# Kernel optimization log

Hardware: AMD Instinct MI355X
Metric: run time of the kernel (lower is better)

The kernel has to match this reference:

```python
import jax, jax.numpy as jnp
import numpy as np

N_NODES = 100000
N_EDGES = 1600000
D_IN = 128
D_HID = 128
D_OUT = 2
BN_EPS = 1e-5


def _sage_conv(x, src, dst, W_l, b_l, W_r):
    # PyG SAGEConv (aggr='mean'): out = lin_l(mean_{j in N(i)} x_j) + lin_r(x_i)
    # messages flow src -> dst
    agg = jax.ops.segment_sum(x[src], dst, num_segments=x.shape[0])
    deg = jax.ops.segment_sum(jnp.ones((src.shape[0],), x.dtype), dst,
                              num_segments=x.shape[0])
    mean = agg / jnp.maximum(deg, 1.0)[:, None]
    return mean @ W_l + b_l + x @ W_r


def _batch_norm(x, gamma, beta):
    # training-mode BatchNorm1d math over the node dimension (biased var)
    mu = jnp.mean(x, axis=0)
    var = jnp.var(x, axis=0)
    return (x - mu) * jax.lax.rsqrt(var + BN_EPS) * gamma + beta


def setup_inputs() -> dict:
    key = jax.random.key(0)
    ks = jax.random.split(key, 10)
    s = lambda d: 1.0 / np.sqrt(d)
    x = jax.random.normal(ks[0], (N_NODES, D_IN), dtype=jnp.float32)
    edge_index = jax.random.randint(ks[1], (2, N_EDGES), 0, N_NODES, dtype=jnp.int64)
    W1l = jax.random.uniform(ks[2], (D_IN, D_HID), jnp.float32, -s(D_IN), s(D_IN))
    b1 = jax.random.uniform(ks[3], (D_HID,), jnp.float32, -s(D_IN), s(D_IN))
    W1r = jax.random.uniform(ks[4], (D_IN, D_HID), jnp.float32, -s(D_IN), s(D_IN))
    W2l = jax.random.uniform(ks[5], (D_HID, D_OUT), jnp.float32, -s(D_HID), s(D_HID))
    b2 = jax.random.uniform(ks[6], (D_OUT,), jnp.float32, -s(D_HID), s(D_HID))
    W2r = jax.random.uniform(ks[7], (D_HID, D_OUT), jnp.float32, -s(D_HID), s(D_HID))
    gamma1 = jnp.ones((D_HID,), jnp.float32)
    beta1 = jnp.zeros((D_HID,), jnp.float32)
    gamma2 = jnp.ones((D_OUT,), jnp.float32)
    beta2 = jnp.zeros((D_OUT,), jnp.float32)
    return {"x": x, "edge_index": edge_index,
            "W1l": W1l, "b1": b1, "W1r": W1r, "gamma1": gamma1, "beta1": beta1,
            "W2l": W2l, "b2": b2, "W2r": W2r, "gamma2": gamma2, "beta2": beta2}


def reference(x, edge_index, W1l, b1, W1r, gamma1, beta1,
              W2l, b2, W2r, gamma2, beta2):
    src, dst = edge_index[0], edge_index[1]
    h = _sage_conv(x, src, dst, W1l, b1, W1r)
    h = _batch_norm(h, gamma1, beta1)
    h = jax.nn.relu(h)
    # dropout in eval mode = identity
    h = _sage_conv(h, src, dst, W2l, b2, W2r)
    h = _batch_norm(h, gamma2, beta2)
    return jax.nn.log_softmax(h, axis=1)
```

## Files before the change

### kernel.cpp

```cpp
#include <hip/hip_runtime.h>
#include <hip/hip_bf16.h>
#include <math.h>


#define DH 128
#define PAD 64
#define CBITS 11
#define CNODES 2048
#define MAXBKT 128
#define BUCKETCAP 65536
#define CHUNK 4096
#define CURSTRIDE 16
#define L1BLOCKS 512

typedef short short8 __attribute__((ext_vector_type(8)));
typedef float float4v __attribute__((ext_vector_type(4)));
typedef float float2v __attribute__((ext_vector_type(2)));
typedef unsigned uint4v __attribute__((ext_vector_type(4)));

template <typename T> static __device__ __forceinline__ float tof(T v);
template <> __device__ __forceinline__ float tof<float>(float v) { return v; }
template <> __device__ __forceinline__ float tof<__hip_bfloat16>(__hip_bfloat16 v) {
  return __bfloat162float(v);
}

static __device__ __forceinline__ short f2bf_s(float f) {
  union { __hip_bfloat16 h; short s; } u;
  u.h = __float2bfloat16(f);
  return u.s;
}

static __device__ __forceinline__ float bf2f(short s) {
  union { unsigned u; float f; } c;
  c.u = ((unsigned)(unsigned short)s) << 16;
  return c.f;
}

static __device__ __forceinline__ float asf(unsigned u) {
  union { unsigned u; float f; } c;
  c.u = u;
  return c.f;
}

__global__ void k_probe(const unsigned* __restrict__ xw,
                        const unsigned* __restrict__ ew,
                        int* __restrict__ flags) {
  int t = threadIdx.x;
  unsigned wx = xw[(size_t)t * 23456 + 7];
  unsigned el = (wx >> 7) & 0xFFu;
  int sx = (el >= 0x60 && el <= 0x85) ? 1 : 0;
  unsigned we = ew[(size_t)t * 12000 + 1];
  int se = (we == 0) ? 1 : 0;
  __shared__ int c[2];
  if (t < 2) c[t] = 0;
  __syncthreads();
  atomicAdd(&c[0], sx);
  atomicAdd(&c[1], se);
  __syncthreads();
  if (t == 0) {
    flags[0] = (c[0] < 192) ? 1 : 0;
    flags[2] = (c[1] > 192) ? 1 : 0;
  }
}

template <typename FT>
static __device__ __forceinline__ void wt_one(const FT* __restrict__ W1l,
                                              const FT* __restrict__ W1r,
                                              short* __restrict__ WT, int idx) {
  int n = idx >> 8, k = idx & 255;
  float v = (k < 128) ? tof(W1l[k * 128 + n]) : tof(W1r[(k - 128) * 128 + n]);
  WT[n * 256 + (k ^ ((n & 7) << 3))] = f2bf_s(v);
}
__global__ void k_xbwt(const void* __restrict__ x, const void* __restrict__ W1l,
                       const void* __restrict__ W1r, const int* __restrict__ flags,
                       __hip_bfloat162* __restrict__ xb, short* __restrict__ WT,
                       int total2) {
  int gi = blockIdx.x * blockDim.x + threadIdx.x;
  bool f32 = flags[0] != 0;
  if (gi < 32768) {
    if (f32) wt_one<float>((const float*)W1l, (const float*)W1r, WT, gi);
    else wt_one<__hip_bfloat16>((const __hip_bfloat16*)W1l, (const __hip_bfloat16*)W1r, WT, gi);
  }
  int i = gi - 32768;
  if (i >= 0 && i < total2) {
    if (f32) {
      float2 v = ((const float2*)x)[i];
      __hip_bfloat162 o;
      o.x = __float2bfloat16(v.x);
      o.y = __float2bfloat16(v.y);
      xb[i] = o;
    } else {
      xb[i] = ((const __hip_bfloat162*)x)[i];
    }
  }
}

template <typename IT>
static __device__ __forceinline__ void part_body(
    const IT* __restrict__ es, const IT* __restrict__ ed,
    int* __restrict__ bktCur, unsigned* __restrict__ bktData,
    int E, int N, int NBKT) {
  __shared__ unsigned pkt[CHUNK];
  __shared__ unsigned char bb[CHUNK];
  __shared__ unsigned ord[CHUNK];
  __shared__ int hist[MAXBKT];
  __shared__ int lstart[MAXBKT + 1];
  __shared__ int cur[MAXBKT];
  __shared__ int gbase[MAXBKT];
  int t = threadIdx.x;
  int e0 = blockIdx.x * CHUNK;
  int nE = min(CHUNK, E - e0);
  if (nE <= 0) return;

  for (int b = t; b < MAXBKT; b += 256) { hist[b] = 0; cur[b] = 0; }
  __syncthreads();
  for (int i = t; i < nE; i += 256) {
    int s = (int)es[e0 + i], d = (int)ed[e0 + i];
    if ((unsigned)s >= (unsigned)N) s = 0;
    if ((unsigned)d >= (unsigned)N) d = 0;
    int b = d >> CBITS;
    bb[i] = (unsigned char)b;
    pkt[i] = ((unsigned)(d & (CNODES - 1)) << 17) | (unsigned)s;
    atomicAdd(&hist[b], 1);
  }
  __syncthreads();
  if (t == 0) {
    int acc = 0;
    for (int b = 0; b < NBKT; ++b) { lstart[b] = acc; acc += hist[b]; }
    lstart[NBKT] = acc;
  }
  __syncthreads();
  if (t < NBKT) {
    int c = hist[t];
    gbase[t] = (c > 0) ? atomicAdd(&bktCur[t * CURSTRIDE], c) : 0;
  }
  __syncthreads();
  for (int i = t; i < nE; i += 256) {
    int b = bb[i];
    int p = atomicAdd(&cur[b], 1);
    ord[lstart[b] + p] = pkt[i];
  }
  __syncthreads();
  for (int i = t; i < nE; i += 256) {
    int lo = 0, hi = NBKT;
    while (hi - lo > 1) { int mid = (lo + hi) >> 1; if (lstart[mid] <= i) lo = mid; else hi = mid; }
    int off = gbase[lo] + (i - lstart[lo]);
    if (off < BUCKETCAP)
      bktData[(size_t)lo * BUCKETCAP + off] = ord[i];
  }
}
__launch_bounds__(256)
__global__ void k_part(const void* __restrict__ ev, const int* __restrict__ flags,
                       int* __restrict__ bktCur, unsigned* __restrict__ bktData,
                       int E, int N, int NBKT) {
  if (flags[2]) part_body<long long>((const long long*)ev, (const long long*)ev + E,
                                     bktCur, bktData, E, N, NBKT);
  else          part_body<int>((const int*)ev, (const int*)ev + E,
                               bktCur, bktData, E, N, NBKT);
}

__launch_bounds__(256)
__global__ void k_build(const unsigned* __restrict__ bktData,
                        const int* __restrict__ bktCur,
                        int* __restrict__ deg_i, int* __restrict__ srcs_pad,
                        int N, int NBKT) {
  __shared__ int deg[256];
  int b = blockIdx.x >> 3;
  int sl = blockIdx.x & 7;
  if (b >= NBKT) return;
  int t = threadIdx.x;
  deg[t] = 0;
  __syncthreads();
  int m = min(bktCur[b * CURSTRIDE], BUCKETCAP);
  const unsigned* pp = bktData + (size_t)b * BUCKETCAP;
  for (int i = t; i < m; i += 256) {
    unsigned u = pp[i];
    int dl = u >> 17;
    if ((dl >> 8) != sl) continue;
    int r = atomicAdd(&deg[dl & 255], 1);
    if (r < PAD) {
      int node = (b << CBITS) + dl;
      srcs_pad[(size_t)node * PAD + r] = (int)(u & 0x1FFFF);
    }
  }
  __syncthreads();
  int node = (b << CBITS) + (sl << 8) + t;
  if (node < N) deg_i[node] = deg[t];
}

static __device__ __forceinline__ void accum8(float2v acc[4], uint4v u) {
#pragma unroll
  for (int i = 0; i < 4; ++i) {
    float2v p;
    p[0] = asf(u[i] << 16);
    p[1] = asf(u[i] & 0xFFFF0000u);
    acc[i] += p;
  }
}
static __device__ __forceinline__ uint4v maskv(uint4v v, int keep) {
  unsigned m = keep ? 0xFFFFFFFFu : 0u;
  uint4v r;
#pragma unroll
  for (int i = 0; i < 4; ++i) r[i] = v[i] & m;
  return r;
}
__launch_bounds__(256)
__global__ void k_gather(const unsigned* __restrict__ xbu,
                         const int* __restrict__ deg_i, const int* __restrict__ srcs_pad,
                         short* __restrict__ meanbs, int N) {
  int node = blockIdx.x * 4 + (threadIdx.x >> 6);
  int lane = threadIdx.x & 63;
  int g = lane >> 4, l = lane & 15;
  if (node >= N) return;
  int dg = deg_i[node];
  int cnt = min(dg, PAD);
  const int* sl = srcs_pad + (size_t)node * PAD;
  int srcv = sl[lane];
  srcv = ((unsigned)srcv < (unsigned)N) ? srcv : 0;
  const uint4v* xv = (const uint4v*)xbu;
  float2v acc[4];
#pragma unroll
  for (int i = 0; i < 4; ++i) acc[i] = (float2v){0.f, 0.f};

  if (cnt > 0) {
    int sA0 = __shfl(srcv, g);
    int sA1 = __shfl(srcv, 4 + g);
    int sA2 = __shfl(srcv, 8 + g);
    int sA3 = __shfl(srcv, 12 + g);
    uint4v a0 = xv[(size_t)sA0 * 16 + l];
    uint4v a1 = xv[(size_t)sA1 * 16 + l];
    uint4v a2 = xv[(size_t)sA2 * 16 + l];
    uint4v a3 = xv[(size_t)sA3 * 16 + l];
    uint4v b0, b1, b2, b3;
    bool hb = cnt > 16;
    if (hb) {
      int sB0 = __shfl(srcv, 16 + g);
      int sB1 = __shfl(srcv, 20 + g);
      int sB2 = __shfl(srcv, 24 + g);
      int sB3 = __shfl(srcv, 28 + g);
      b0 = xv[(size_t)sB0 * 16 + l];
      b1 = xv[(size_t)sB1 * 16 + l];
      b2 = xv[(size_t)sB2 * 16 + l];
      b3 = xv[(size_t)sB3 * 16 + l];
    }
    a0 = maskv(a0, g < cnt);
    a1 = maskv(a1, 4 + g < cnt);
    a2 = maskv(a2, 8 + g < cnt);
    a3 = maskv(a3, 12 + g < cnt);
    accum8(acc, a0);
    accum8(acc, a1);
    accum8(acc, a2);
    accum8(acc, a3);
    if (hb) {
      b0 = maskv(b0, 16 + g < cnt);
      b1 = maskv(b1, 20 + g < cnt);
      b2 = maskv(b2, 24 + g < cnt);
      b3 = maskv(b3, 28 + g < cnt);
      accum8(acc, b0);
      accum8(acc, b1);
      accum8(acc, b2);
      accum8(acc, b3);
    }
    for (int j = 32; j < cnt; j += 16) {
      int s0 = __shfl(srcv, j + g);
      int s1 = __shfl(srcv, j + 4 + g);
      int s2 = __shfl(srcv, j + 8 + g);
      int s3 = __shfl(srcv, j + 12 + g);
      uint4v v0 = xv[(size_t)s0 * 16 + l];
      uint4v v1 = xv[(size_t)s1 * 16 + l];
      uint4v v2 = xv[(size_t)s2 * 16 + l];
      uint4v v3 = xv[(size_t)s3 * 16 + l];
      v0 = maskv(v0, j + g < cnt);
      v1 = maskv(v1, j + 4 + g < cnt);
      v2 = maskv(v2, j + 8 + g < cnt);
      v3 = maskv(v3, j + 12 + g < cnt);
      accum8(acc, v0);
      accum8(acc, v1);
      accum8(acc, v2);
      accum8(acc, v3);
    }
  }

#pragma unroll
  for (int i = 0; i < 4; ++i) {
#pragma unroll
    for (int c = 0; c < 2; ++c) {
      acc[i][c] += __shfl_xor(acc[i][c], 16);
      acc[i][c] += __shfl_xor(acc[i][c], 32);
    }
  }
  if (g == 0) {
    float invd = 1.0f / fmaxf((float)dg, 1.0f);
    short8 o;
#pragma unroll
    for (int i = 0; i < 4; ++i) {
      o[2 * i]     = f2bf_s(acc[i][0] * invd);
      o[2 * i + 1] = f2bf_s(acc[i][1] * invd);
    }
    *(short8*)(meanbs + (size_t)node * DH + l * 8) = o;
  }
}

template <typename FT>
static __device__ __forceinline__ void layer1_body(
    const short* __restrict__ meanbs, const short* __restrict__ xbs,
    const short* __restrict__ WTs, const FT* __restrict__ b1,
    __hip_bfloat16* __restrict__ h1, float* __restrict__ st1,
    int N, int ntiles) {
  __shared__ short ldsWT[32768];
  int t = threadIdx.x;
  {
    const uint4v* src = (const uint4v*)WTs;
    uint4v* dst = (uint4v*)ldsWT;
#pragma unroll
    for (int i = 0; i < 16; ++i) dst[t + i * 256] = src[t + i * 256];
  }
  __syncthreads();

  int w = t >> 6;
  int lane = t & 63;
  int m = lane & 15;
  int quad = lane >> 4;
  int xm = (m & 7) << 3;

  float bs[8], bq[8];
#pragma unroll
  for (int c = 0; c < 8; ++c) { bs[c] = 0.f; bq[c] = 0.f; }
  float bias[8];
#pragma unroll
  for (int c = 0; c < 8; ++c) bias[c] = tof(b1[c * 16 + m]);

  for (int tt = blockIdx.x; tt < ntiles; tt += gridDim.x) {
    int rowbase = tt * 64 + w * 16;
    int arowc = min(rowbase + m, N - 1);

    short8 afrag[8];
    const short* mr = meanbs + (size_t)arowc * DH;
#pragma unroll
    for (int kt = 0; kt < 4; ++kt)
      afrag[kt] = *(const short8*)(mr + kt * 32 + quad * 8);
    const short* xr = xbs + (size_t)arowc * DH;
#pragma unroll
    for (int kt = 0; kt < 4; ++kt)
      afrag[4 + kt] = *(const short8*)(xr + kt * 32 + quad * 8);

    float4v acc[8];
#pragma unroll
    for (int c = 0; c < 8; ++c) acc[c] = (float4v){0.f, 0.f, 0.f, 0.f};

#pragma unroll
    for (int kt = 0; kt < 8; ++kt) {
      int koff = (kt * 32 + quad * 8) ^ xm;
#pragma unroll
      for (int c = 0; c < 8; ++c) {
        short8 b = *(const short8*)(ldsWT + (c * 16 + m) * 256 + koff);
        acc[c] = __builtin_amdgcn_mfma_f32_16x16x32_bf16(afrag[kt], b, acc[c], 0, 0, 0);
      }
    }

#pragma unroll
    for (int c = 0; c < 8; ++c) {
      int col = c * 16 + m;
#pragma unroll
      for (int r = 0; r < 4; ++r) {
        int ro = rowbase + quad * 4 + r;
        float v = acc[c][r] + bias[c];
        if (ro < N) {
          h1[(size_t)ro * DH + col] = __float2bfloat16(v);
          bs[c] += v;
          bq[c] += v * v;
        }
      }
    }
  }

  __syncthreads();
  float* lsum = (float*)ldsWT;
  float* lsq  = lsum + 512;
#pragma unroll
  for (int c = 0; c < 8; ++c) {
    float s = bs[c], q = bq[c];
    s += __shfl_xor(s, 16); s += __shfl_xor(s, 32);
    q += __shfl_xor(q, 16); q += __shfl_xor(q, 32);
    if (quad == 0) { lsum[w * 128 + c * 16 + m] = s; lsq[w * 128 + c * 16 + m] = q; }
  }
  __syncthreads();
  if (t < 128) {
    float s = lsum[0 * 128 + t] + lsum[1 * 128 + t] + lsum[2 * 128 + t] + lsum[3 * 128 + t];
    float q = lsq[0 * 128 + t] + lsq[1 * 128 + t] + lsq[2 * 128 + t] + lsq[3 * 128 + t];
    unsafeAtomicAdd(&st1[t], s);
    unsafeAtomicAdd(&st1[128 + t], q);
  }
}
__launch_bounds__(256)
__global__ void k_layer1(const short* __restrict__ meanbs, const short* __restrict__ xbs,
                         const short* __restrict__ WTs, const void* __restrict__ b1,
                         const int* __restrict__ flags,
                         __hip_bfloat16* __restrict__ h1, float* __restrict__ st1,
                         int N, int ntiles) {
  if (flags[0])
    layer1_body<float>(meanbs, xbs, WTs, (const float*)b1, h1, st1, N, ntiles);
  else
    layer1_body<__hip_bfloat16>(meanbs, xbs, WTs, (const __hip_bfloat16*)b1,
                                h1, st1, N, ntiles);
}

template <typename FT>
static __device__ __forceinline__ void zr_body(
    const short* __restrict__ h1s, const float* __restrict__ stats1,
    const FT* __restrict__ g1, const FT* __restrict__ be1,
    const FT* __restrict__ W2l, const FT* __restrict__ W2r,
    float4* __restrict__ zr, int N) {
  __shared__ float sc[128], sh[128];
  int t = threadIdx.x;
  if (t < 128) {
    float invN = 1.0f / (float)N;
    float mu = stats1[t] * invN;
    float var = stats1[128 + t] * invN - mu * mu;
    float a = tof(g1[t]) * rsqrtf(var + 1e-5f);
    sc[t] = a;
    sh[t] = tof(be1[t]) - mu * a;
  }
  __syncthreads();
  int lane = t & 63, w = t >> 6;
  int g = lane >> 4, l = lane & 15;
  int f0 = l * 8;
  float scl[8], shl[8], wl0[8], wl1[8], wr0[8], wr1[8];
#pragma unroll
  for (int j = 0; j < 8; ++j) {
    int f = f0 + j;
    scl[j] = sc[f];
    shl[j] = sh[f];
    wl0[j] = tof(W2l[f * 2 + 0]);
    wl1[j] = tof(W2l[f * 2 + 1]);
    wr0[j] = tof(W2r[f * 2 + 0]);
    wr1[j] = tof(W2r[f * 2 + 1]);
  }
  int gw = blockIdx.x * 4 + w;
  int nw = gridDim.x * 4;
  for (int base = gw * 4; base < N; base += nw * 4) {
    int node = base + g;
    if (node < N) {
      short8 hv = *(const short8*)(h1s + (size_t)node * DH + f0);
      float z0 = 0.f, z1 = 0.f, r0 = 0.f, r1 = 0.f;
#pragma unroll
      for (int j = 0; j < 8; ++j) {
        float v = fmaxf(bf2f(hv[j]) * scl[j] + shl[j], 0.0f);
        z0 += v * wl0[j];
        z1 += v * wl1[j];
        r0 += v * wr0[j];
        r1 += v * wr1[j];
      }
#pragma unroll
      for (int off = 8; off >= 1; off >>= 1) {
        z0 += __shfl_xor(z0, off);
        z1 += __shfl_xor(z1, off);
        r0 += __shfl_xor(r0, off);
        r1 += __shfl_xor(r1, off);
      }
      if (l == 0) zr[node] = make_float4(z0, z1, r0, r1);
    }
  }
}
__launch_bounds__(256)
__global__ void k_zr(const __hip_bfloat16* __restrict__ h1, const float* __restrict__ st1,
                     const void* g1, const void* be1, const void* W2l, const void* W2r,
                     const int* __restrict__ flags, float4* __restrict__ zr, int N) {
  if (flags[0])
    zr_body<float>((const short*)h1, st1, (const float*)g1, (const float*)be1,
                   (const float*)W2l, (const float*)W2r, zr, N);
  else
    zr_body<__hip_bfloat16>((const short*)h1, st1, (const __hip_bfloat16*)g1,
                            (const __hip_bfloat16*)be1,
                            (const __hip_bfloat16*)W2l, (const __hip_bfloat16*)W2r, zr, N);
}

template <typename FT>
static __device__ __forceinline__ void h2_body(
    const float2* __restrict__ z2, const int* __restrict__ deg_i,
    const int* __restrict__ srcs_pad, const FT* __restrict__ b2,
    float2* __restrict__ h2, float* __restrict__ stats2, int N) {
  int lane = threadIdx.x & 63, w = threadIdx.x >> 6;
  int g = lane >> 4, l = lane & 15;
  float bs0 = 0.f, bs1 = 0.f, bq0 = 0.f, bq1 = 0.f;
  float bb0 = tof(b2[0]), bb1 = tof(b2[1]);
  int gw = blockIdx.x * 4 + w;
  int nw = gridDim.x * 4;
  for (int base = gw * 4; base < N; base += nw * 4) {
    int node = base + g;
    float za = 0.f, zb = 0.f;
    int dg_true = 0;
    if (node < N) {
      dg_true = deg_i[node];
      int cnt = min(dg_true, PAD);
      const int* sl = srcs_pad + (size_t)node * PAD;
      for (int j = l; j < cnt; j += 16) {
        int sj = sl[j];
        sj = ((unsigned)sj < (unsigned)N) ? sj : 0;
        float2 v = z2[2 * sj];
        za += v.x;
        zb += v.y;
      }
    }
#pragma unroll
    for (int off = 8; off >= 1; off >>= 1) {
      za += __shfl_xor(za, off);
      zb += __shfl_xor(zb, off);
    }
    if (node < N && l == 0) {
      float dg = fmaxf((float)dg_true, 1.0f);
      float2 rw = z2[2 * node + 1];
      float h0 = za / dg + rw.x + bb0;
      float h1v = zb / dg + rw.y + bb1;
      h2[node] = make_float2(h0, h1v);
      bs0 += h0; bs1 += h1v; bq0 += h0 * h0; bq1 += h1v * h1v;
    }
  }
  bs0 += __shfl_xor(bs0, 16); bs0 += __shfl_xor(bs0, 32);
  bs1 += __shfl_xor(bs1, 16); bs1 += __shfl_xor(bs1, 32);
  bq0 += __shfl_xor(bq0, 16); bq0 += __shfl_xor(bq0, 32);
  bq1 += __shfl_xor(bq1, 16); bq1 += __shfl_xor(bq1, 32);
  __shared__ float red[4][4];
  if (lane == 0) { red[w][0] = bs0; red[w][1] = bs1; red[w][2] = bq0; red[w][3] = bq1; }
  __syncthreads();
  if (threadIdx.x < 4) {
    float a = red[0][threadIdx.x] + red[1][threadIdx.x] +
              red[2][threadIdx.x] + red[3][threadIdx.x];
    unsafeAtomicAdd(&stats2[threadIdx.x], a);
  }
}
__launch_bounds__(256)
__global__ void k_h2(const float4* __restrict__ zr, const int* __restrict__ deg_i,
                     const int* __restrict__ srcs_pad, const void* b2,
                     const int* __restrict__ flags,
                     float2* __restrict__ h2, float* __restrict__ stats2, int N) {
  if (flags[0])
    h2_body<float>((const float2*)zr, deg_i, srcs_pad, (const float*)b2, h2, stats2, N);
  else
    h2_body<__hip_bfloat16>((const float2*)zr, deg_i, srcs_pad,
                            (const __hip_bfloat16*)b2, h2, stats2, N);
}

template <typename FT>
static __device__ __forceinline__ void out_body(
    const float2* __restrict__ h2, const float* __restrict__ stats2,
    const FT* __restrict__ g2, const FT* __restrict__ be2,
    void* __restrict__ out, int N) {
  int i = blockIdx.x * blockDim.x + threadIdx.x;
  if (i >= N) return;
  float invN = 1.0f / (float)N;
  float mu0 = stats2[0] * invN, mu1 = stats2[1] * invN;
  float v0 = stats2[2] * invN - mu0 * mu0;
  float v1 = stats2[3] * invN - mu1 * mu1;
  float r0 = rsqrtf(v0 + 1e-5f), r1 = rsqrtf(v1 + 1e-5f);
  float2 h = h2[i];
  float y0 = (h.x - mu0) * r0 * tof(g2[0]) + tof(be2[0]);
  float y1 = (h.y - mu1) * r1 * tof(g2[1]) + tof(be2[1]);
  float mx = fmaxf(y0, y1);
  float lse = mx + logf(expf(y0 - mx) + expf(y1 - mx));
  float o0 = y0 - lse, o1 = y1 - lse;
  if (sizeof(FT) == 4) {
    ((float2*)out)[i] = make_float2(o0, o1);
  } else {
    __hip_bfloat162 o;
    o.x = __float2bfloat16(o0);
    o.y = __float2bfloat16(o1);
    ((__hip_bfloat162*)out)[i] = o;
  }
}
__global__ void k_out(const float2* __restrict__ h2, const float* __restrict__ stats2,
                      const void* g2, const void* be2, const int* __restrict__ flags,
                      void* __restrict__ out, int N) {
  if (flags[0]) out_body<float>(h2, stats2, (const float*)g2, (const float*)be2, out, N);
  else out_body<__hip_bfloat16>(h2, stats2, (const __hip_bfloat16*)g2,
                                (const __hip_bfloat16*)be2, out, N);
}

extern "C" void kernel_launch(void* const* d_in, const int* in_sizes, int n_in,
                              void* d_out, int out_size, void* d_ws, size_t ws_size,
                              hipStream_t stream) {
  int ix = 0, ie = 1, iW1l = 2, ib1 = 3, iW1r = 4, ig1 = 5, ibe1 = 6,
      iW2l = 7, ib2 = 8, iW2r = 9, ig2 = 10, ibe2 = 11;
  if (n_in == 12) {
    int best = -1, second = -1;
    for (int i = 0; i < 12; ++i) {
      if (best < 0 || in_sizes[i] > in_sizes[best]) { second = best; best = i; }
      else if (second < 0 || in_sizes[i] > in_sizes[second]) second = i;
    }
    ix = best; ie = second;
    int c16384 = 0, c128 = 0, c256 = 0, c2 = 0;
    for (int i = 0; i < 12; ++i) {
      if (i == ix || i == ie) continue;
      int s = in_sizes[i];
      if (s == 16384) { if (c16384++ == 0) iW1l = i; else iW1r = i; }
      else if (s == 128) { if (c128 == 0) ib1 = i; else if (c128 == 1) ig1 = i; else ibe1 = i; c128++; }
      else if (s == 256) { if (c256++ == 0) iW2l = i; else iW2r = i; }
      else { if (c2 == 0) ib2 = i; else if (c2 == 1) ig2 = i; else ibe2 = i; c2++; }
    }
  }

  const void* x   = d_in[ix];
  const void* ev  = d_in[ie];
  const void* W1l = d_in[iW1l];
  const void* b1  = d_in[ib1];
  const void* W1r = d_in[iW1r];
  const void* g1  = d_in[ig1];
  const void* be1 = d_in[ibe1];
  const void* W2l = d_in[iW2l];
  const void* b2  = d_in[ib2];
  const void* W2r = d_in[iW2r];
  const void* g2  = d_in[ig2];
  const void* be2 = d_in[ibe2];

  int N = in_sizes[ix] / DH;
  int E = in_sizes[ie] / 2;
  int nb = (N + 63) / 64;
  int NBKT = (N + CNODES - 1) >> CBITS;
  if (NBKT > MAXBKT) NBKT = MAXBKT;

  int grid1 = (nb < L1BLOCKS) ? nb : L1BLOCKS;
  int nblkp = (E + CHUNK - 1) / CHUNK;

  char* ws = (char*)d_ws;
  size_t off = 0;
  auto alloc = [&](size_t b) { size_t o = off; off += (b + 255) & ~(size_t)255; return o; };
  size_t o_st1   = alloc(256 * 4);
  size_t o_st2   = alloc(4 * 4);
  size_t o_cur   = alloc((size_t)MAXBKT * CURSTRIDE * 4);
  size_t zlen = off;
  size_t o_bdat  = alloc((size_t)NBKT * BUCKETCAP * 4);
  size_t o_degi  = alloc((size_t)N * 4);
  size_t o_srcs  = alloc((size_t)N * PAD * 4);
  size_t o_xb    = alloc((size_t)N * DH * 2);
  size_t o_mean  = alloc((size_t)N * DH * 2);
  size_t o_h1    = alloc((size_t)N * DH * 2);
  size_t o_wt    = alloc(256 * 128 * 2);
  size_t o_zr    = alloc((size_t)N * 16);
  size_t o_h2    = alloc((size_t)N * 8);
  size_t o_flg   = alloc(64);

  float* st1  = (float*)(ws + o_st1);
  float* st2  = (float*)(ws + o_st2);
  int* bktCur = (int*)(ws + o_cur);
  unsigned* bktData = (unsigned*)(ws + o_bdat);
  int* deg_i  = (int*)(ws + o_degi);
  int* srcs   = (int*)(ws + o_srcs);
  __hip_bfloat162* xb = (__hip_bfloat162*)(ws + o_xb);
  short* meanb = (short*)(ws + o_mean);
  __hip_bfloat16* h1 = (__hip_bfloat16*)(ws + o_h1);
  short* WT   = (short*)(ws + o_wt);
  float4* zrp = (float4*)(ws + o_zr);
  float2* h2p = (float2*)(ws + o_h2);
  int* flags  = (int*)(ws + o_flg);

  hipMemsetAsync(d_ws, 0, zlen, stream);

  int total2 = N * 64;
  k_probe<<<1, 256, 0, stream>>>((const unsigned*)x, (const unsigned*)ev, flags);
  k_xbwt<<<(total2 + 32768 + 255) / 256, 256, 0, stream>>>(x, W1l, W1r, flags, xb, WT, total2);
  k_part<<<nblkp, 256, 0, stream>>>(ev, flags, bktCur, bktData, E, N, NBKT);
  k_build<<<NBKT * 8, 256, 0, stream>>>(bktData, bktCur, deg_i, srcs, N, NBKT);
  k_gather<<<(N + 3) / 4, 256, 0, stream>>>((const unsigned*)xb, deg_i, srcs, meanb, N);
  k_layer1<<<grid1, 256, 0, stream>>>(meanb, (const short*)xb, WT, b1,
                                      flags, h1, st1, N, nb);
  k_zr<<<2048, 256, 0, stream>>>(h1, st1, g1, be1, W2l, W2r, flags, zrp, N);
  k_h2<<<2048, 256, 0, stream>>>(zrp, deg_i, srcs, b2, flags, h2p, st2, N);
  k_out<<<(N + 255) / 256, 256, 0, stream>>>(h2p, st2, g2, be2, flags, d_out, N);
}
```

Baseline: 346.6 us.

## Merge prep kernels and fuse tail stages into one cooperative kernel

Merges the x/weight bf16 conversion and the edge partitioning into a single launch by splitting the block range between the two jobs. Replaces the three tail kernels (zr, h2, output) with one cooperative kernel that uses grid-wide syncs between phases, and falls back to the separate launches if the cooperative launch fails. This is meant to cut launch gaps and small-kernel overhead. The cost is grid sync latency and a fixed grid of 1024 blocks that may change occupancy for the zr and h2 phases.

```diff
diff --git a/kernel.cpp b/kernel.cpp
--- a/kernel.cpp
+++ b/kernel.cpp
@@ -1,6 +1,9 @@
 #include <hip/hip_runtime.h>
+#include <hip/hip_cooperative_groups.h>
 #include <hip/hip_bf16.h>
 #include <math.h>
+
+namespace cg = cooperative_groups;
 
 
 #define DH 128
@@ -71,12 +74,11 @@
   float v = (k < 128) ? tof(W1l[k * 128 + n]) : tof(W1r[(k - 128) * 128 + n]);
   WT[n * 256 + (k ^ ((n & 7) << 3))] = f2bf_s(v);
 }
-__global__ void k_xbwt(const void* __restrict__ x, const void* __restrict__ W1l,
-                       const void* __restrict__ W1r, const int* __restrict__ flags,
-                       __hip_bfloat162* __restrict__ xb, short* __restrict__ WT,
-                       int total2) {
-  int gi = blockIdx.x * blockDim.x + threadIdx.x;
-  bool f32 = flags[0] != 0;
+static __device__ __forceinline__ void xbwt_one(
+    const void* __restrict__ x, const void* __restrict__ W1l,
+    const void* __restrict__ W1r, bool f32,
+    __hip_bfloat162* __restrict__ xb, short* __restrict__ WT,
+    int gi, int total2) {
   if (gi < 32768) {
     if (f32) wt_one<float>((const float*)W1l, (const float*)W1r, WT, gi);
     else wt_one<__hip_bfloat16>((const __hip_bfloat16*)W1l, (const __hip_bfloat16*)W1r, WT, gi);
@@ -149,14 +151,24 @@
       bktData[(size_t)lo * BUCKETCAP + off] = ord[i];
   }
 }
+
 __launch_bounds__(256)
-__global__ void k_part(const void* __restrict__ ev, const int* __restrict__ flags,
+__global__ void k_prep(const void* __restrict__ x, const void* __restrict__ W1l,
+                       const void* __restrict__ W1r, const void* __restrict__ ev,
+                       const int* __restrict__ flags,
+                       __hip_bfloat162* __restrict__ xb, short* __restrict__ WT,
+                       int total2,
                        int* __restrict__ bktCur, unsigned* __restrict__ bktData,
-                       int E, int N, int NBKT) {
-  if (flags[2]) part_body<long long>((const long long*)ev, (const long long*)ev + E,
-                                     bktCur, bktData, E, N, NBKT);
-  else          part_body<int>((const int*)ev, (const int*)ev + E,
-                               bktCur, bktData, E, N, NBKT);
+                       int E, int N, int NBKT, int nblkp) {
+  if ((int)blockIdx.x < nblkp) {
+    if (flags[2]) part_body<long long>((const long long*)ev, (const long long*)ev + E,
+                                       bktCur, bktData, E, N, NBKT);
+    else          part_body<int>((const int*)ev, (const int*)ev + E,
+                                 bktCur, bktData, E, N, NBKT);
+  } else {
+    int gi = (blockIdx.x - nblkp) * blockDim.x + threadIdx.x;
+    xbwt_one(x, W1l, W1r, flags[0] != 0, xb, WT, gi, total2);
+  }
 }
 
 __launch_bounds__(256)
@@ -542,12 +554,10 @@
 }
 
 template <typename FT>
-static __device__ __forceinline__ void out_body(
+static __device__ __forceinline__ void out_one(
     const float2* __restrict__ h2, const float* __restrict__ stats2,
     const FT* __restrict__ g2, const FT* __restrict__ be2,
-    void* __restrict__ out, int N) {
-  int i = blockIdx.x * blockDim.x + threadIdx.x;
-  if (i >= N) return;
+    void* __restrict__ out, int i, int N) {
   float invN = 1.0f / (float)N;
   float mu0 = stats2[0] * invN, mu1 = stats2[1] * invN;
   float v0 = stats2[2] * invN - mu0 * mu0;
@@ -571,9 +581,53 @@
 __global__ void k_out(const float2* __restrict__ h2, const float* __restrict__ stats2,
                       const void* g2, const void* be2, const int* __restrict__ flags,
                       void* __restrict__ out, int N) {
-  if (flags[0]) out_body<float>(h2, stats2, (const float*)g2, (const float*)be2, out, N);
-  else out_body<__hip_bfloat16>(h2, stats2, (const __hip_bfloat16*)g2,
-                                (const __hip_bfloat16*)be2, out, N);
+  int i = blockIdx.x * blockDim.x + threadIdx.x;
+  if (i >= N) return;
+  if (flags[0]) out_one<float>(h2, stats2, (const float*)g2, (const float*)be2, out, i, N);
+  else out_one<__hip_bfloat16>(h2, stats2, (const __hip_bfloat16*)g2,
+                               (const __hip_bfloat16*)be2, out, i, N);
+}
+
+__launch_bounds__(256, 4)
+__global__ void k_tail(const __hip_bfloat16* __restrict__ h1,
+                       const float* __restrict__ st1,
+                       const void* g1, const void* be1,
+                       const void* W2l, const void* W2r,
+                       const void* b2, const void* g2, const void* be2,
+                       const int* __restrict__ flags,
+                       const int* __restrict__ deg_i,
+                       const int* __restrict__ srcs_pad,
+                       float4* __restrict__ zrp, float2* __restrict__ h2p,
+                       float* __restrict__ st2, void* __restrict__ out, int N) {
+  cg::grid_group grid = cg::this_grid();
+  bool f32 = flags[0] != 0;
+
+  if (f32)
+    zr_body<float>((const short*)h1, st1, (const float*)g1, (const float*)be1,
+                   (const float*)W2l, (const float*)W2r, zrp, N);
+  else
+    zr_body<__hip_bfloat16>((const short*)h1, st1, (const __hip_bfloat16*)g1,
+                            (const __hip_bfloat16*)be1,
+                            (const __hip_bfloat16*)W2l, (const __hip_bfloat16*)W2r,
+                            zrp, N);
+  __threadfence();
+  grid.sync();
+
+  if (f32)
+    h2_body<float>((const float2*)zrp, deg_i, srcs_pad, (const float*)b2,
+                   h2p, st2, N);
+  else
+    h2_body<__hip_bfloat16>((const float2*)zrp, deg_i, srcs_pad,
+                            (const __hip_bfloat16*)b2, h2p, st2, N);
+  __threadfence();
+  grid.sync();
+
+  int stride = gridDim.x * blockDim.x;
+  for (int i = blockIdx.x * blockDim.x + threadIdx.x; i < N; i += stride) {
+    if (f32) out_one<float>(h2p, st2, (const float*)g2, (const float*)be2, out, i, N);
+    else out_one<__hip_bfloat16>(h2p, st2, (const __hip_bfloat16*)g2,
+                                 (const __hip_bfloat16*)be2, out, i, N);
+  }
 }
 
 extern "C" void kernel_launch(void* const* d_in, const int* in_sizes, int n_in,
@@ -620,6 +674,8 @@
 
   int grid1 = (nb < L1BLOCKS) ? nb : L1BLOCKS;
   int nblkp = (E + CHUNK - 1) / CHUNK;
+  int total2 = N * 64;
+  int nxb = (total2 + 32768 + 255) / 256;
 
   char* ws = (char*)d_ws;
   size_t off = 0;
@@ -655,15 +711,37 @@
 
   hipMemsetAsync(d_ws, 0, zlen, stream);
 
-  int total2 = N * 64;
   k_probe<<<1, 256, 0, stream>>>((const unsigned*)x, (const unsigned*)ev, flags);
-  k_xbwt<<<(total2 + 32768 + 255) / 256, 256, 0, stream>>>(x, W1l, W1r, flags, xb, WT, total2);
-  k_part<<<nblkp, 256, 0, stream>>>(ev, flags, bktCur, bktData, E, N, NBKT);
+  k_prep<<<nblkp + nxb, 256, 0, stream>>>(x, W1l, W1r, ev, flags, xb, WT, total2,
+                                          bktCur, bktData, E, N, NBKT, nblkp);
   k_build<<<NBKT * 8, 256, 0, stream>>>(bktData, bktCur, deg_i, srcs, N, NBKT);
   k_gather<<<(N + 3) / 4, 256, 0, stream>>>((const unsigned*)xb, deg_i, srcs, meanb, N);
   k_layer1<<<grid1, 256, 0, stream>>>(meanb, (const short*)xb, WT, b1,
                                       flags, h1, st1, N, nb);
-  k_zr<<<2048, 256, 0, stream>>>(h1, st1, g1, be1, W2l, W2r, flags, zrp, N);
-  k_h2<<<2048, 256, 0, stream>>>(zrp, deg_i, srcs, b2, flags, h2p, st2, N);
-  k_out<<<(N + 255) / 256, 256, 0, stream>>>(h2p, st2, g2, be2, flags, d_out, N);
-}
+
+  {
+    const __hip_bfloat16* a_h1 = h1;
+    const float* a_st1 = st1;
+    const void* a_g1 = g1;  const void* a_be1 = be1;
+    const void* a_W2l = W2l; const void* a_W2r = W2r;
+    const void* a_b2 = b2;  const void* a_g2 = g2;  const void* a_be2 = be2;
+    const int* a_flags = flags;
+    const int* a_degi = deg_i;
+    const int* a_srcs = srcs;
+    float4* a_zrp = zrp;
+    float2* a_h2p = h2p;
+    float* a_st2 = st2;
+    void* a_out = d_out;
+    int a_N = N;
+    void* args[] = {&a_h1, &a_st1, &a_g1, &a_be1, &a_W2l, &a_W2r, &a_b2,
+                    &a_g2, &a_be2, &a_flags, &a_degi, &a_srcs,
+                    &a_zrp, &a_h2p, &a_st2, &a_out, &a_N};
+    hipError_t cerr = hipLaunchCooperativeKernel(
+        reinterpret_cast<void*>(k_tail), dim3(1024), dim3(256), args, 0, stream);
+    if (cerr != hipSuccess) {
+      k_zr<<<2048, 256, 0, stream>>>(h1, st1, g1, be1, W2l, W2r, flags, zrp, N);
+      k_h2<<<2048, 256, 0, stream>>>(zrp, deg_i, srcs, b2, flags, h2p, st2, N);
+      k_out<<<(N + 255) / 256, 256, 0, stream>>>(h2p, st2, g2, be2, flags, d_out, N);
+    }
+  }
+}
```

Result: slower. 748.6 us (+116.0%).
